# Optimization experiments

Measured on AMD Instinct MI355X. Metric: run time of the kernel, lower is better.

## Reference

```python
import jax, jax.numpy as jnp
import numpy as np

ALPHA, BETA, GAMMA = 2.0, 2.0, 1.0
EPS = 1e-8  # torch F.cosine_similarity eps
B, T, D = 64, 1024, 256


def setup_inputs() -> dict:
    key = jax.random.key(0)
    k1, k2, k3 = jax.random.split(key, 3)
    f_v = jax.random.normal(k1, (B, T, D), dtype=jnp.float32)
    f_a = jax.random.normal(k2, (B, T, D), dtype=jnp.float32)
    labels = jax.random.randint(k3, (B,), 0, 2, dtype=jnp.int64)
    return {"f_v": f_v, "f_a": f_a, "labels": labels}


def _normalize(x):
    n = jnp.sqrt(jnp.sum(x * x, axis=-1, keepdims=True))
    return x / jnp.maximum(n, EPS)


def reference(f_v, f_a, labels):
    b, t, _ = f_v.shape
    vn = _normalize(f_v)  # [B,T,D]
    an = _normalize(f_a)  # [B,T,D]

    # --- per-timestep aligned-pair term ---
    cos_bt = jnp.sum(vn * an, axis=-1)  # [B,T] cosine sim
    d_bt = 1.0 - cos_bt                  # cosine distance
    pos_mask = (labels == 0).astype(f_v.dtype)[:, None]  # [B,1]
    neg_mask = 1.0 - pos_mask
    loss_pos = ALPHA * jnp.sum(d_bt * pos_mask)
    cnt_pos = jnp.sum(pos_mask) * t
    loss_neg = BETA * jnp.sum((1.0 - d_bt) * neg_mask)  # (1-d) == cos
    cnt_neg = jnp.sum(neg_mask) * t

    # --- cross-sample term: for i != j, (1 - mean_t d_ij) = mean_t cos(v_i_t, a_j_t) ---
    cross_cos = jnp.einsum('itd,jtd->ij', vn, an) / t  # [B,B] mean over T
    offdiag = 1.0 - jnp.eye(b, dtype=f_v.dtype)
    loss_neg = loss_neg + GAMMA * jnp.sum(cross_cos * offdiag)
    cnt_neg = cnt_neg + b * (b - 1)

    loss = jnp.where(cnt_pos > 0, loss_pos / jnp.maximum(cnt_pos, 1.0), 0.0)
    loss = loss + jnp.where(cnt_neg > 0, loss_neg / jnp.maximum(cnt_neg, 1.0), 0.0)
    return loss
```

## Files before the change

kernel.cpp:

```cpp
#include <hip/hip_runtime.h>

constexpr int Bn = 64;
constexpr int Tn = 1024;
constexpr int Dn = 256;

constexpr int TPB    = 256;
constexpr int NBLK   = 512;
constexpr int TPERB  = Tn / NBLK;
constexpr int KC     = 64;
constexpr int NCHUNK = Dn / KC;
constexpr int PITCH  = KC + 4;

__device__ __forceinline__ float dot4(const float4& a, const float4& b) {
    return a.x * b.x + a.y * b.y + a.z * b.z + a.w * b.w;
}

__global__ __launch_bounds__(TPB, 2)
void cmfm_main(const float* __restrict__ fv, const float* __restrict__ fa,
               const int* __restrict__ labels, float* __restrict__ acc) {
    __shared__ __align__(16) float Vs[Bn][PITCH];
    __shared__ __align__(16) float As[KC][PITCH];
    __shared__ float rvs[Bn];
    __shared__ float ras[Bn];
    __shared__ float wred[3][TPB / 64];

    const int tid = threadIdx.x;
    const int row = tid >> 2;
    const int q   = tid & 3;
    const int tx  = tid & 15;
    const int ty  = tid >> 4;
    const int i0  = ty * 4;
    const int j0  = tx * 4;

    const int lab = labels[row];

    const float4* __restrict__ fv4 = reinterpret_cast<const float4*>(fv);
    const float4* __restrict__ fa4 = reinterpret_cast<const float4*>(fa);

    float C[4][4] = {};
    float pos_acc = 0.f, neg_acc = 0.f;

    for (int tt = 0; tt < TPERB; ++tt) {
        const int t = blockIdx.x * TPERB + tt;
        const size_t base = ((size_t)row * Tn + t) * (Dn / 4);

        float S[4][4] = {};
        float sqv = 0.f, sqa = 0.f, dva = 0.f;

        for (int c = 0; c < NCHUNK; ++c) {
            const size_t f4base = base + (size_t)c * (KC / 4);
            float4 v4[4], a4[4];
            #pragma unroll
            for (int k = 0; k < 4; ++k) {
                const int f4i = q + 4 * k;
                v4[k] = fv4[f4base + f4i];
                a4[k] = fa4[f4base + f4i];
            }
            #pragma unroll
            for (int k = 0; k < 4; ++k) {
                sqv += dot4(v4[k], v4[k]);
                sqa += dot4(a4[k], a4[k]);
                dva += dot4(v4[k], a4[k]);
                const int d = (q + 4 * k) * 4;
                *reinterpret_cast<float4*>(&Vs[row][d]) = v4[k];
                As[d + 0][row] = a4[k].x;
                As[d + 1][row] = a4[k].y;
                As[d + 2][row] = a4[k].z;
                As[d + 3][row] = a4[k].w;
            }
            __syncthreads();

            #pragma unroll
            for (int d4 = 0; d4 < KC / 4; ++d4) {
                float va[4][4], ab[4][4];
                #pragma unroll
                for (int r = 0; r < 4; ++r) {
                    float4 v = *reinterpret_cast<const float4*>(&Vs[i0 + r][d4 * 4]);
                    va[r][0] = v.x; va[r][1] = v.y; va[r][2] = v.z; va[r][3] = v.w;
                }
                #pragma unroll
                for (int m = 0; m < 4; ++m) {
                    float4 a = *reinterpret_cast<const float4*>(&As[d4 * 4 + m][j0]);
                    ab[m][0] = a.x; ab[m][1] = a.y; ab[m][2] = a.z; ab[m][3] = a.w;
                }
                #pragma unroll
                for (int dd = 0; dd < 4; ++dd)
                    #pragma unroll
                    for (int r = 0; r < 4; ++r)
                        #pragma unroll
                        for (int s = 0; s < 4; ++s)
                            S[r][s] = fmaf(va[r][dd], ab[dd][s], S[r][s]);
            }
            __syncthreads();
        }

        sqv += __shfl_xor(sqv, 1); sqv += __shfl_xor(sqv, 2);
        sqa += __shfl_xor(sqa, 1); sqa += __shfl_xor(sqa, 2);
        dva += __shfl_xor(dva, 1); dva += __shfl_xor(dva, 2);
        const float rv = 1.f / fmaxf(sqrtf(sqv), 1e-8f);
        const float ra = 1.f / fmaxf(sqrtf(sqa), 1e-8f);
        if (q == 0) {
            rvs[row] = rv;
            ras[row] = ra;
            const float cosd = dva * rv * ra;
            if (lab == 0) pos_acc += 1.f - cosd;
            else          neg_acc += cosd;
        }
        __syncthreads();

        float rvv[4], raa[4];
        #pragma unroll
        for (int r = 0; r < 4; ++r) rvv[r] = rvs[i0 + r];
        #pragma unroll
        for (int s = 0; s < 4; ++s) raa[s] = ras[j0 + s];
        #pragma unroll
        for (int r = 0; r < 4; ++r)
            #pragma unroll
            for (int s = 0; s < 4; ++s)
                C[r][s] = fmaf(rvv[r] * raa[s], S[r][s], C[r][s]);
        __syncthreads();
    }

    float od = 0.f;
    #pragma unroll
    for (int r = 0; r < 4; ++r)
        #pragma unroll
        for (int s = 0; s < 4; ++s) od += C[r][s];
    if (ty == tx) {
        #pragma unroll
        for (int r = 0; r < 4; ++r) od -= C[r][r];
    }

    #pragma unroll
    for (int off = 1; off < 64; off <<= 1) {
        pos_acc += __shfl_xor(pos_acc, off);
        neg_acc += __shfl_xor(neg_acc, off);
        od      += __shfl_xor(od, off);
    }
    const int wave = tid >> 6;
    const int lane = tid & 63;
    if (lane == 0) {
        wred[0][wave] = pos_acc;
        wred[1][wave] = neg_acc;
        wred[2][wave] = od;
    }
    __syncthreads();
    if (tid == 0) {
        float p = 0.f, n = 0.f, o = 0.f;
        #pragma unroll
        for (int w = 0; w < TPB / 64; ++w) { p += wred[0][w]; n += wred[1][w]; o += wred[2][w]; }
        atomicAdd(&acc[0], p);
        atomicAdd(&acc[1], n);
        atomicAdd(&acc[2], o);
    }
}

__global__ void cmfm_final(const int* __restrict__ labels, const float* __restrict__ acc,
                           float* __restrict__ out) {
    if (threadIdx.x == 0) {
        int npos = 0;
        for (int i = 0; i < Bn; ++i) npos += (labels[i] == 0);
        const float pos_sum   = acc[0];
        const float neg_sum   = acc[1];
        const float cross_sum = acc[2];

        const float cnt_pos = (float)npos * (float)Tn;
        const float cnt_neg = (float)(Bn - npos) * (float)Tn + (float)Bn * (float)(Bn - 1);

        float loss = 0.f;
        if (npos > 0) loss += 2.0f * pos_sum / cnt_pos;
        loss += (2.0f * neg_sum + 1.0f * cross_sum / (float)Tn) / cnt_neg;
        out[0] = loss;
    }
}

extern "C" void kernel_launch(void* const* d_in, const int* in_sizes, int n_in,
                              void* d_out, int out_size, void* d_ws, size_t ws_size,
                              hipStream_t stream) {
    const float* fv     = (const float*)d_in[0];
    const float* fa     = (const float*)d_in[1];
    const int*   labels = (const int*)d_in[2];
    float* acc = (float*)d_ws;
    float* out = (float*)d_out;

    hipMemsetAsync(acc, 0, 3 * sizeof(float), stream);
    cmfm_main<<<NBLK, TPB, 0, stream>>>(fv, fa, labels, acc);
    cmfm_final<<<1, 64, 0, stream>>>(labels, acc, out);
}
```

Baseline: 167.3 us.

## Compute cross-sample Gram with bf16 MFMA, one timestep per block

Replaces the fp32 FMA register-tiled 64x64 Gram product per timestep with bf16 MFMA 32x32x16 instructions on a swizzled LDS layout. The grid becomes one block per timestep, and each block does the D dimension in two halves. The atomic accumulators are spread across separate cache lines. The intent is to cut the ALU-bound inner product cost and LDS bank conflicts. The risk is precision loss from rounding the inputs to bf16 in the cross term.

```diff
diff --git a/kernel.cpp b/kernel.cpp
--- a/kernel.cpp
+++ b/kernel.cpp
@@ -4,131 +4,126 @@
 constexpr int Tn = 1024;
 constexpr int Dn = 256;
 
-constexpr int TPB    = 256;
-constexpr int NBLK   = 512;
-constexpr int TPERB  = Tn / NBLK;
-constexpr int KC     = 64;
-constexpr int NCHUNK = Dn / KC;
-constexpr int PITCH  = KC + 4;
+constexpr int TPB  = 256;
+constexpr int NBLK = Tn;
+
+using short8 = __attribute__((ext_vector_type(8))) short;
+using f32x16 = __attribute__((ext_vector_type(16))) float;
 
 __device__ __forceinline__ float dot4(const float4& a, const float4& b) {
     return a.x * b.x + a.y * b.y + a.z * b.z + a.w * b.w;
 }
 
-__global__ __launch_bounds__(TPB, 2)
+__device__ __forceinline__ unsigned int bfbits(float x) {
+    unsigned int u = __builtin_bit_cast(unsigned int, x);
+    return (u + 0x7FFFu + ((u >> 16) & 1u)) >> 16;
+}
+__device__ __forceinline__ unsigned int pack_bf2(float lo, float hi) {
+    return bfbits(lo) | (bfbits(hi) << 16);
+}
+
+__global__ __launch_bounds__(TPB, 4)
 void cmfm_main(const float* __restrict__ fv, const float* __restrict__ fa,
-               const int* __restrict__ labels, float* __restrict__ acc) {
-    __shared__ __align__(16) float Vs[Bn][PITCH];
-    __shared__ __align__(16) float As[KC][PITCH];
-    __shared__ float rvs[Bn];
-    __shared__ float ras[Bn];
+               const int* __restrict__ labels, float* __restrict__ acc)
+{
+    __shared__ __align__(16) unsigned int Vb[Bn * 64];
+    __shared__ __align__(16) unsigned int Ab[Bn * 64];
+    __shared__ float rvs[Bn], ras[Bn];
     __shared__ float wred[3][TPB / 64];
 
-    const int tid = threadIdx.x;
-    const int row = tid >> 2;
-    const int q   = tid & 3;
-    const int tx  = tid & 15;
-    const int ty  = tid >> 4;
-    const int i0  = ty * 4;
-    const int j0  = tx * 4;
+    const int tid  = threadIdx.x;
+    const int row  = tid >> 2;
+    const int q    = tid & 3;
+    const int lane = tid & 63;
+    const int wave = tid >> 6;
 
     const int lab = labels[row];
-
     const float4* __restrict__ fv4 = reinterpret_cast<const float4*>(fv);
     const float4* __restrict__ fa4 = reinterpret_cast<const float4*>(fa);
 
-    float C[4][4] = {};
-    float pos_acc = 0.f, neg_acc = 0.f;
+    const int t = blockIdx.x;
+    const size_t base = ((size_t)row * Tn + t) * (Dn / 4);
 
-    for (int tt = 0; tt < TPERB; ++tt) {
-        const int t = blockIdx.x * TPERB + tt;
-        const size_t base = ((size_t)row * Tn + t) * (Dn / 4);
+    const int i0   = (wave >> 1) * 32;
+    const int j0   = (wave & 1) * 32;
+    const int mrow = lane & 31;
+    const int half = lane >> 5;
+    const int rsx  = mrow & 15;
+    const unsigned vrb = (unsigned)(i0 + mrow) * 64;
+    const unsigned arb = (unsigned)(j0 + mrow) * 64;
 
-        float S[4][4] = {};
-        float sqv = 0.f, sqa = 0.f, dva = 0.f;
+    const int wsx = row & 15;
+    const unsigned wrb = (unsigned)row * 64;
 
-        for (int c = 0; c < NCHUNK; ++c) {
-            const size_t f4base = base + (size_t)c * (KC / 4);
-            float4 v4[4], a4[4];
-            #pragma unroll
-            for (int k = 0; k < 4; ++k) {
-                const int f4i = q + 4 * k;
-                v4[k] = fv4[f4base + f4i];
-                a4[k] = fa4[f4base + f4i];
-            }
-            #pragma unroll
-            for (int k = 0; k < 4; ++k) {
-                sqv += dot4(v4[k], v4[k]);
-                sqa += dot4(a4[k], a4[k]);
-                dva += dot4(v4[k], a4[k]);
-                const int d = (q + 4 * k) * 4;
-                *reinterpret_cast<float4*>(&Vs[row][d]) = v4[k];
-                As[d + 0][row] = a4[k].x;
-                As[d + 1][row] = a4[k].y;
-                As[d + 2][row] = a4[k].z;
-                As[d + 3][row] = a4[k].w;
-            }
-            __syncthreads();
+    f32x16 C;
+    #pragma unroll
+    for (int r = 0; r < 16; ++r) C[r] = 0.f;
 
-            #pragma unroll
-            for (int d4 = 0; d4 < KC / 4; ++d4) {
-                float va[4][4], ab[4][4];
-                #pragma unroll
-                for (int r = 0; r < 4; ++r) {
-                    float4 v = *reinterpret_cast<const float4*>(&Vs[i0 + r][d4 * 4]);
-                    va[r][0] = v.x; va[r][1] = v.y; va[r][2] = v.z; va[r][3] = v.w;
-                }
-                #pragma unroll
-                for (int m = 0; m < 4; ++m) {
-                    float4 a = *reinterpret_cast<const float4*>(&As[d4 * 4 + m][j0]);
-                    ab[m][0] = a.x; ab[m][1] = a.y; ab[m][2] = a.z; ab[m][3] = a.w;
-                }
-                #pragma unroll
-                for (int dd = 0; dd < 4; ++dd)
-                    #pragma unroll
-                    for (int r = 0; r < 4; ++r)
-                        #pragma unroll
-                        for (int s = 0; s < 4; ++s)
-                            S[r][s] = fmaf(va[r][dd], ab[dd][s], S[r][s]);
-            }
-            __syncthreads();
+    float sqv = 0.f, sqa = 0.f, dva = 0.f;
+    float rv = 0.f, ra = 0.f;
+
+    #pragma unroll
+    for (int h = 0; h < 2; ++h) {
+        float4 v4[8], a4[8];
+        #pragma unroll
+        for (int k = 0; k < 8; ++k) v4[k] = fv4[base + q + 4 * (8 * h + k)];
+        #pragma unroll
+        for (int k = 0; k < 8; ++k) a4[k] = fa4[base + q + 4 * (8 * h + k)];
+
+        #pragma unroll
+        for (int k = 0; k < 8; ++k) {
+            sqv += dot4(v4[k], v4[k]);
+            sqa += dot4(a4[k], a4[k]);
+            dva += dot4(v4[k], a4[k]);
         }
 
-        sqv += __shfl_xor(sqv, 1); sqv += __shfl_xor(sqv, 2);
-        sqa += __shfl_xor(sqa, 1); sqa += __shfl_xor(sqa, 2);
-        dva += __shfl_xor(dva, 1); dva += __shfl_xor(dva, 2);
-        const float rv = 1.f / fmaxf(sqrtf(sqv), 1e-8f);
-        const float ra = 1.f / fmaxf(sqrtf(sqa), 1e-8f);
-        if (q == 0) {
-            rvs[row] = rv;
-            ras[row] = ra;
-            const float cosd = dva * rv * ra;
-            if (lab == 0) pos_acc += 1.f - cosd;
-            else          neg_acc += cosd;
+        #pragma unroll
+        for (int k = 0; k < 8; ++k) {
+            const int d4l  = q + 4 * k;
+            const int slot = d4l >> 1;
+            const unsigned idx = wrb + (unsigned)(((slot ^ wsx) << 2) + (d4l & 1) * 2);
+            uint2 pv, pa;
+            pv.x = pack_bf2(v4[k].x, v4[k].y); pv.y = pack_bf2(v4[k].z, v4[k].w);
+            pa.x = pack_bf2(a4[k].x, a4[k].y); pa.y = pack_bf2(a4[k].z, a4[k].w);
+            *reinterpret_cast<uint2*>(&Vb[idx]) = pv;
+            *reinterpret_cast<uint2*>(&Ab[idx]) = pa;
+        }
+
+        if (h == 1) {
+            sqv += __shfl_xor(sqv, 1); sqv += __shfl_xor(sqv, 2);
+            sqa += __shfl_xor(sqa, 1); sqa += __shfl_xor(sqa, 2);
+            dva += __shfl_xor(dva, 1); dva += __shfl_xor(dva, 2);
+            rv = 1.f / fmaxf(sqrtf(sqv), 1e-8f);
+            ra = 1.f / fmaxf(sqrtf(sqa), 1e-8f);
+            if (q == 0) { rvs[row] = rv; ras[row] = ra; }
         }
         __syncthreads();
 
-        float rvv[4], raa[4];
         #pragma unroll
-        for (int r = 0; r < 4; ++r) rvv[r] = rvs[i0 + r];
-        #pragma unroll
-        for (int s = 0; s < 4; ++s) raa[s] = ras[j0 + s];
-        #pragma unroll
-        for (int r = 0; r < 4; ++r)
-            #pragma unroll
-            for (int s = 0; s < 4; ++s)
-                C[r][s] = fmaf(rvv[r] * raa[s], S[r][s], C[r][s]);
-        __syncthreads();
+        for (int s = 0; s < 8; ++s) {
+            const int slotl = s * 2 + half;
+            const short8 av = *reinterpret_cast<const short8*>(&Vb[vrb + ((slotl ^ rsx) << 2)]);
+            const short8 bv = *reinterpret_cast<const short8*>(&Ab[arb + ((slotl ^ rsx) << 2)]);
+            C = __builtin_amdgcn_mfma_f32_32x32x16_bf16(av, bv, C, 0, 0, 0);
+        }
+        if (h == 0) __syncthreads();
     }
 
+    float pos_acc = 0.f, neg_acc = 0.f;
+    if (q == 0) {
+        const float cosd = dva * rv * ra;
+        if (lab == 0) pos_acc = 1.f - cosd;
+        else          neg_acc = cosd;
+    }
+
+    const float raj = ras[j0 + mrow];
     float od = 0.f;
     #pragma unroll
-    for (int r = 0; r < 4; ++r)
-        #pragma unroll
-        for (int s = 0; s < 4; ++s) od += C[r][s];
-    if (ty == tx) {
-        #pragma unroll
-        for (int r = 0; r < 4; ++r) od -= C[r][r];
+    for (int r = 0; r < 16; ++r) {
+        const int ri = (r & 3) + 8 * (r >> 2) + 4 * half;
+        float c = C[r];
+        if (i0 == j0 && ri == mrow) c = 0.f;
+        od += rvs[i0 + ri] * raj * c;
     }
 
     #pragma unroll
@@ -137,21 +132,15 @@
         neg_acc += __shfl_xor(neg_acc, off);
         od      += __shfl_xor(od, off);
     }
-    const int wave = tid >> 6;
-    const int lane = tid & 63;
-    if (lane == 0) {
-        wred[0][wave] = pos_acc;
-        wred[1][wave] = neg_acc;
-        wred[2][wave] = od;
-    }
+    if (lane == 0) { wred[0][wave] = pos_acc; wred[1][wave] = neg_acc; wred[2][wave] = od; }
     __syncthreads();
     if (tid == 0) {
         float p = 0.f, n = 0.f, o = 0.f;
         #pragma unroll
         for (int w = 0; w < TPB / 64; ++w) { p += wred[0][w]; n += wred[1][w]; o += wred[2][w]; }
-        atomicAdd(&acc[0], p);
-        atomicAdd(&acc[1], n);
-        atomicAdd(&acc[2], o);
+        atomicAdd(&acc[0],  p);
+        atomicAdd(&acc[16], n);
+        atomicAdd(&acc[32], o);
     }
 }
 
@@ -161,8 +150,8 @@
         int npos = 0;
         for (int i = 0; i < Bn; ++i) npos += (labels[i] == 0);
         const float pos_sum   = acc[0];
-        const float neg_sum   = acc[1];
-        const float cross_sum = acc[2];
+        const float neg_sum   = acc[16];
+        const float cross_sum = acc[32];
 
         const float cnt_pos = (float)npos * (float)Tn;
         const float cnt_neg = (float)(Bn - npos) * (float)Tn + (float)Bn * (float)(Bn - 1);
@@ -183,7 +172,7 @@
     float* acc = (float*)d_ws;
     float* out = (float*)d_out;
 
-    hipMemsetAsync(acc, 0, 3 * sizeof(float), stream);
+    hipMemsetAsync(acc, 0, 64 * sizeof(float), stream);
     cmfm_main<<<NBLK, TPB, 0, stream>>>(fv, fa, labels, acc);
     cmfm_final<<<1, 64, 0, stream>>>(labels, acc, out);
 }
```

New measurement: 161.0 us. 1.04x faster.
